# Performance work log

Hardware: AMD Instinct MI355X
Metric: run time of the kernel (lower is better)

The kernel has to match this reference:

```python
import jax, jax.numpy as jnp
import numpy as np

P1, P2 = 100003, 1009  # spatial hash primes from the torch source
D = 16  # block_dim (stage-3 BLOCK_DIM)

FACE_OFFSETS = jnp.array([[-1,0,0],[1,0,0],[0,-1,0],[0,1,0],[0,0,-1],[0,0,1]], dtype=jnp.int32)
NEIGHBOR_OFFSETS = jnp.array([
    [-1,0,0],[1,0,0],[0,-1,0],[0,1,0],[0,0,-1],[0,0,1],
    [-1,-1,0],[-1,1,0],[1,-1,0],[1,1,0],
    [-1,0,-1],[-1,0,1],[1,0,-1],[1,0,1],
    [0,-1,-1],[0,-1,1],[0,1,-1],[0,1,1],
    [-1,-1,-1],[-1,-1,1],[-1,1,-1],[-1,1,1],
    [1,-1,-1],[1,-1,1],[1,1,-1],[1,1,1]], dtype=jnp.int32)


def _face_dists_flat(d):
    # [d^3, 6] distance of each in-block voxel to the 6 block faces, in [0,1]
    lin = jnp.linspace(0.0, 1.0, d)
    gx, gy, gz = jnp.meshgrid(lin, lin, lin, indexing='ij')
    return jnp.stack([gx, 1.0 - gx, gy, 1.0 - gy, gz, 1.0 - gz], axis=-1).reshape(-1, 6)


def _match(xyz, offsets):
    # xyz: [N,3] int32 block coords of one batch; offsets: [K,3]
    # returns [N,K] bool: does a block exist at xyz+offset (hash sort + searchsorted)
    n = xyz.shape[0]
    keys = xyz[:, 0] * P1 + xyz[:, 1] * P2 + xyz[:, 2]
    sorted_keys = jnp.sort(keys)
    nb = xyz[:, None, :] + offsets[None, :, :]               # [N,K,3]
    nbk = (nb[..., 0] * P1 + nb[..., 1] * P2 + nb[..., 2]).reshape(-1)
    pos = jnp.clip(jnp.searchsorted(sorted_keys, nbk), 0, n - 1)
    return (sorted_keys[pos] == nbk).reshape(n, offsets.shape[0])


def setup_inputs() -> dict:
    key = jax.random.key(0)
    # [B, N, 3] block coords (batch dim explicit, equal per-batch layout)
    coords = jax.random.randint(key, (4, 2048, 3), 0, 64, dtype=jnp.int32)
    return {"coords": coords}


def reference(coords):
    face_flat = _face_dists_flat(D)                           # [D^3, 6]
    has_nb = jax.vmap(lambda x: _match(x, FACE_OFFSETS))(coords)       # [B,N,6]
    # face without a neighbor keeps its boundary distance; else distance 1.0
    prior = jnp.min(jnp.where(has_nb[:, :, None, :], 1.0, face_flat[None, None, :, :]), axis=-1)  # [B,N,D^3]
    occ = jax.vmap(lambda x: _match(x, NEIGHBOR_OFFSETS))(coords).astype(jnp.float32)             # [B,N,26]
    return prior, occ
```

## Files before the change

kernel.cpp:

```cpp
#include <hip/hip_runtime.h>


#define B 4
#define N 2048
#define PPB 8
#define BLOCKS_PER_BATCH (N / PPB)
#define BM_WORDS 8192
#define PRIOR_ELEMS (4ull * 2048ull * 4096ull)

static __device__ __constant__ int NB_OFF[26][3] = {
    {-1,0,0},{1,0,0},{0,-1,0},{0,1,0},{0,0,-1},{0,0,1},
    {-1,-1,0},{-1,1,0},{1,-1,0},{1,1,0},
    {-1,0,-1},{-1,0,1},{1,0,-1},{1,0,1},
    {0,-1,-1},{0,-1,1},{0,1,-1},{0,1,1},
    {-1,-1,-1},{-1,-1,1},{-1,1,-1},{-1,1,1},
    {1,-1,-1},{1,-1,1},{1,1,-1},{1,1,1}
};

__device__ __forceinline__ bool bm_test(const unsigned* bm, int x, int y, int z) {
    if (((x | y | z) & ~63) != 0) return false;
    unsigned idx = ((unsigned)x << 12) | ((unsigned)y << 6) | (unsigned)z;
    return (bm[idx >> 5] >> (idx & 31u)) & 1u;
}

__global__ void __launch_bounds__(256, 4)
fused_kernel(const int* __restrict__ coords, float* __restrict__ out) {
    __shared__ unsigned bm[BM_WORDS];
    __shared__ unsigned char fex[PPB][6];

    const int tid = threadIdx.x;
    const int blk = blockIdx.x;
    const int b = blk / BLOCKS_PER_BATCH;
    const int p0 = (blk % BLOCKS_PER_BATCH) * PPB;
    const int* cb = coords + b * N * 3;

    for (int i = tid; i < BM_WORDS; i += 256) bm[i] = 0u;
    __syncthreads();

    for (int i = tid; i < N; i += 256) {
        int x = cb[3 * i + 0];
        int y = cb[3 * i + 1];
        int z = cb[3 * i + 2];
        unsigned idx = ((unsigned)x << 12) | ((unsigned)y << 6) | (unsigned)z;
        atomicOr(&bm[idx >> 5], 1u << (idx & 31u));
    }
    __syncthreads();

    if (tid < PPB * 6) {
        int p = tid / 6, f = tid % 6;
        int x = cb[3 * (p0 + p) + 0];
        int y = cb[3 * (p0 + p) + 1];
        int z = cb[3 * (p0 + p) + 2];
        fex[p][f] = bm_test(bm, x + NB_OFF[f][0], y + NB_OFF[f][1], z + NB_OFF[f][2]) ? 1 : 0;
    }
    if (tid < PPB * 26) {
        int p = tid / 26, k = tid % 26;
        int x = cb[3 * (p0 + p) + 0];
        int y = cb[3 * (p0 + p) + 1];
        int z = cb[3 * (p0 + p) + 2];
        float hit = bm_test(bm, x + NB_OFF[k][0], y + NB_OFF[k][1], z + NB_OFF[k][2]) ? 1.0f : 0.0f;
        out[PRIOR_ELEMS + (size_t)(b * N + p0) * 26 + tid] = hit;
    }
    __syncthreads();

    const float inv15 = 1.0f / 15.0f;
    #pragma unroll
    for (int p = 0; p < PPB; ++p) {
        bool nxm = fex[p][0], nxp = fex[p][1];
        bool nym = fex[p][2], nyp = fex[p][3];
        bool nzm = fex[p][4], nzp = fex[p][5];
        float4* outp = (float4*)(out + (size_t)(b * N + p0 + p) * 4096);
        #pragma unroll
        for (int j = 0; j < 4; ++j) {
            int v4 = j * 256 + tid;
            int v = v4 * 4;
            float gx = (float)((v >> 8) & 15) * inv15;
            float gy = (float)((v >> 4) & 15) * inv15;
            int iz0 = v & 15;
            float m = 1.0f;
            if (!nxm) m = fminf(m, gx);
            if (!nxp) m = fminf(m, 1.0f - gx);
            if (!nym) m = fminf(m, gy);
            if (!nyp) m = fminf(m, 1.0f - gy);
            float r[4];
            #pragma unroll
            for (int k = 0; k < 4; ++k) {
                float gz = (float)(iz0 + k) * inv15;
                float mm = m;
                if (!nzm) mm = fminf(mm, gz);
                if (!nzp) mm = fminf(mm, 1.0f - gz);
                r[k] = mm;
            }
            outp[v4] = make_float4(r[0], r[1], r[2], r[3]);
        }
    }
}

extern "C" void kernel_launch(void* const* d_in, const int* in_sizes, int n_in,
                              void* d_out, int out_size, void* d_ws, size_t ws_size,
                              hipStream_t stream) {
    const int* coords = (const int*)d_in[0];
    float* out = (float*)d_out;
    fused_kernel<<<B * N / PPB, 256, 0, stream>>>(coords, out);
}
```

Before: 137.7 us.

## Split fused kernel into occupancy kernel and LDS-free prior writer

Splits the fused kernel in two. The first builds the per-batch shared-memory bitmap only once per 32 points and writes the 26-neighbor occupancy. The second reads the first six occupancy flags and streams the prior volume with no shared memory, allowing higher occupancy. This removes the redundant bitmap rebuild done in every block of the old kernel and frees LDS for the bandwidth-bound write. The cost is an extra launch and a global-memory round trip for the face flags.

Result: no change. 139.5 us (+1.4%).

```diff
diff --git a/kernel.cpp b/kernel.cpp
--- a/kernel.cpp
+++ b/kernel.cpp
@@ -3,10 +3,12 @@
 
 #define B 4
 #define N 2048
-#define PPB 8
-#define BLOCKS_PER_BATCH (N / PPB)
 #define BM_WORDS 8192
 #define PRIOR_ELEMS (4ull * 2048ull * 4096ull)
+
+#define K1_BPB 64
+#define K1_PTS (N / K1_BPB)
+#define PPB2 4
 
 static __device__ __constant__ int NB_OFF[26][3] = {
     {-1,0,0},{1,0,0},{0,-1,0},{0,1,0},{0,0,-1},{0,0,1},
@@ -24,14 +26,13 @@
 }
 
 __global__ void __launch_bounds__(256, 4)
-fused_kernel(const int* __restrict__ coords, float* __restrict__ out) {
+occ_kernel(const int* __restrict__ coords, float* __restrict__ out) {
     __shared__ unsigned bm[BM_WORDS];
-    __shared__ unsigned char fex[PPB][6];
 
     const int tid = threadIdx.x;
     const int blk = blockIdx.x;
-    const int b = blk / BLOCKS_PER_BATCH;
-    const int p0 = (blk % BLOCKS_PER_BATCH) * PPB;
+    const int b = blk / K1_BPB;
+    const int p0 = (blk % K1_BPB) * K1_PTS;
     const int* cb = coords + b * N * 3;
 
     for (int i = tid; i < BM_WORDS; i += 256) bm[i] = 0u;
@@ -46,30 +47,29 @@
     }
     __syncthreads();
 
-    if (tid < PPB * 6) {
-        int p = tid / 6, f = tid % 6;
-        int x = cb[3 * (p0 + p) + 0];
-        int y = cb[3 * (p0 + p) + 1];
-        int z = cb[3 * (p0 + p) + 2];
-        fex[p][f] = bm_test(bm, x + NB_OFF[f][0], y + NB_OFF[f][1], z + NB_OFF[f][2]) ? 1 : 0;
+    for (int i = tid; i < K1_PTS * 26; i += 256) {
+        int p = i / 26, k = i % 26;
+        int x = cb[3 * (p0 + p) + 0] + NB_OFF[k][0];
+        int y = cb[3 * (p0 + p) + 1] + NB_OFF[k][1];
+        int z = cb[3 * (p0 + p) + 2] + NB_OFF[k][2];
+        out[PRIOR_ELEMS + (size_t)(b * N + p0 + p) * 26 + k] =
+            bm_test(bm, x, y, z) ? 1.0f : 0.0f;
     }
-    if (tid < PPB * 26) {
-        int p = tid / 26, k = tid % 26;
-        int x = cb[3 * (p0 + p) + 0];
-        int y = cb[3 * (p0 + p) + 1];
-        int z = cb[3 * (p0 + p) + 2];
-        float hit = bm_test(bm, x + NB_OFF[k][0], y + NB_OFF[k][1], z + NB_OFF[k][2]) ? 1.0f : 0.0f;
-        out[PRIOR_ELEMS + (size_t)(b * N + p0) * 26 + tid] = hit;
-    }
-    __syncthreads();
+}
 
+__global__ void __launch_bounds__(256, 8)
+prior_kernel(const float* __restrict__ occ, float* __restrict__ out) {
+    const int tid = threadIdx.x;
+    const int gp0 = blockIdx.x * PPB2;
     const float inv15 = 1.0f / 15.0f;
+
     #pragma unroll
-    for (int p = 0; p < PPB; ++p) {
-        bool nxm = fex[p][0], nxp = fex[p][1];
-        bool nym = fex[p][2], nyp = fex[p][3];
-        bool nzm = fex[p][4], nzp = fex[p][5];
-        float4* outp = (float4*)(out + (size_t)(b * N + p0 + p) * 4096);
+    for (int p = 0; p < PPB2; ++p) {
+        const float* o = occ + (size_t)(gp0 + p) * 26;
+        bool nxm = o[0] != 0.0f, nxp = o[1] != 0.0f;
+        bool nym = o[2] != 0.0f, nyp = o[3] != 0.0f;
+        bool nzm = o[4] != 0.0f, nzp = o[5] != 0.0f;
+        float4* outp = (float4*)(out + (size_t)(gp0 + p) * 4096);
         #pragma unroll
         for (int j = 0; j < 4; ++j) {
             int v4 = j * 256 + tid;
@@ -101,5 +101,6 @@
                               hipStream_t stream) {
     const int* coords = (const int*)d_in[0];
     float* out = (float*)d_out;
-    fused_kernel<<<B * N / PPB, 256, 0, stream>>>(coords, out);
+    occ_kernel<<<B * K1_BPB, 256, 0, stream>>>(coords, out);
+    prior_kernel<<<B * N / PPB2, 256, 0, stream>>>(out + PRIOR_ELEMS, out);
 }
```
